# Optimization experiments

Measured on AMD Instinct MI355X. Metric: run time of the kernel, lower is better.

## Reference

```python
import jax, jax.numpy as jnp
import numpy as np

N, E, DIN, DE, D, L = 100000, 600000, 64, 8, 128, 5
BN_EPS = 1e-5


def setup_inputs() -> dict:
    key = jax.random.key(0)
    ks = jax.random.split(key, 10)
    s = 0.05
    return {
        "x": jax.random.normal(ks[0], (N, DIN), jnp.float32),
        "edge_index": jax.random.randint(ks[1], (2, E), 0, N, dtype=jnp.int64) if jax.config.jax_enable_x64 else jax.random.randint(ks[1], (2, E), 0, N),
        "edge_attr": jax.random.normal(ks[2], (E, DE), jnp.float32),
        "Wn": jax.random.normal(ks[3], (DIN, D), jnp.float32) * s,
        "bn0": jnp.zeros((D,), jnp.float32),
        "We": jax.random.normal(ks[4], (L, DE, D), jnp.float32) * s,
        "bee": jnp.zeros((L, D), jnp.float32),
        "W1": jax.random.normal(ks[5], (L, D, 2 * D), jnp.float32) * s,
        "b1": jnp.zeros((L, 2 * D), jnp.float32),
        "g1": jnp.ones((L, 2 * D), jnp.float32),
        "bt1": jnp.zeros((L, 2 * D), jnp.float32),
        "W2": jax.random.normal(ks[6], (L, 2 * D, D), jnp.float32) * s,
        "b2": jnp.zeros((L, D), jnp.float32),
        "eps": jnp.zeros((L,), jnp.float32),
        "gamma": jnp.ones((L, D), jnp.float32),
        "beta": jnp.zeros((L, D), jnp.float32),
    }


def _bn(z, g, b):
    # BatchNorm1d training-mode forward (biased variance over the node axis)
    mu = jnp.mean(z, axis=0)
    var = jnp.mean((z - mu) ** 2, axis=0)
    return g * (z - mu) * jax.lax.rsqrt(var + BN_EPS) + b


def reference(x, edge_index, edge_attr, Wn, bn0, We, bee, W1, b1, g1, bt1, W2, b2, eps, gamma, beta):
    h = x @ Wn + bn0  # node encoder: [N, D]
    src, dst = edge_index[0], edge_index[1]
    for l in range(L):
        ee = edge_attr @ We[l] + bee[l]              # [E, D] edge embedding
        msg = jax.nn.relu(h[src] + ee)               # gather + relu
        agg = jax.ops.segment_sum(msg, dst, num_segments=N)  # scatter-add
        z = (1.0 + eps[l]) * h + agg                 # GIN root update
        z = jax.nn.relu(_bn(z @ W1[l] + b1[l], g1[l], bt1[l]))  # MLP hidden
        z = z @ W2[l] + b2[l]                        # MLP out
        z = _bn(z, gamma[l], beta[l])                # outer BatchNorm
        if l < L - 1:
            z = jax.nn.relu(z)                       # relu on all but last layer
        h = z
    return h  # JK='last'
```

## Files before the change

### kernel.cpp

```cpp
#include <hip/hip_runtime.h>
#include <hip/hip_bf16.h>

#define N_NODES 100000
#define N_EDGES 600000
#define DIN 64
#define DE 8
#define D 128
#define TWO_D 256
#define L_LAYERS 5
#define BN_EPS 1e-5f

#define SCAN_B 256
#define SCAN_NB ((N_NODES + SCAN_B - 1) / SCAN_B)

typedef unsigned short u16;
typedef unsigned int u32;
typedef __attribute__((ext_vector_type(8))) short short8;
typedef __attribute__((ext_vector_type(4))) float f32x4;

__device__ inline u16 f2bf(float f) {
    __hip_bfloat16 h = __float2bfloat16(f);
    return *reinterpret_cast<u16*>(&h);
}
__device__ inline float bf2f(u16 u) {
    union { u32 i; float f; } v;
    v.i = ((u32)u) << 16;
    return v.f;
}
__device__ inline float bfLo(u32 v) {
    union { u32 i; float f; } u;
    u.i = v << 16;
    return u.f;
}
__device__ inline float bfHi(u32 v) {
    union { u32 i; float f; } u;
    u.i = v & 0xffff0000u;
    return u.f;
}
__device__ inline u32 packbf(float a, float b) {
    return (u32)f2bf(a) | ((u32)f2bf(b) << 16);
}


__global__ void hist_kernel(const int* __restrict__ dst, int* __restrict__ deg) {
    int i = blockIdx.x * blockDim.x + threadIdx.x;
    if (i < N_EDGES) atomicAdd(&deg[dst[i]], 1);
}

__global__ void scan_partial_kernel(const int* __restrict__ deg, int* __restrict__ blocksum) {
    __shared__ int red[SCAN_B];
    int tid = threadIdx.x;
    int i = blockIdx.x * SCAN_B + tid;
    red[tid] = (i < N_NODES) ? deg[i] : 0;
    __syncthreads();
    for (int off = SCAN_B / 2; off > 0; off >>= 1) {
        if (tid < off) red[tid] += red[tid + off];
        __syncthreads();
    }
    if (tid == 0) blocksum[blockIdx.x] = red[0];
}

__global__ void scan_blocks_kernel(int* __restrict__ blocksum, int* __restrict__ total) {
    __shared__ int sh[512];
    int tid = threadIdx.x;
    int v = (tid < SCAN_NB) ? blocksum[tid] : 0;
    sh[tid] = v;
    __syncthreads();
    for (int off = 1; off < 512; off <<= 1) {
        int w = (tid >= off) ? sh[tid - off] : 0;
        __syncthreads();
        sh[tid] += w;
        __syncthreads();
    }
    if (tid < SCAN_NB) blocksum[tid] = sh[tid] - v;
    if (tid == 511) *total = sh[511];
}

__global__ void scan_apply_kernel(const int* __restrict__ deg, const int* __restrict__ blocksum,
                                  const int* __restrict__ total, int* __restrict__ rowptr,
                                  int* __restrict__ cursor) {
    __shared__ int sh[SCAN_B];
    int tid = threadIdx.x;
    int i = blockIdx.x * SCAN_B + tid;
    int v = (i < N_NODES) ? deg[i] : 0;
    sh[tid] = v;
    __syncthreads();
    for (int off = 1; off < SCAN_B; off <<= 1) {
        int w = (tid >= off) ? sh[tid - off] : 0;
        __syncthreads();
        sh[tid] += w;
        __syncthreads();
    }
    if (i < N_NODES) {
        int p = blocksum[blockIdx.x] + sh[tid] - v;
        rowptr[i] = p;
        cursor[i] = p;
    }
    if (i == N_NODES - 1) rowptr[N_NODES] = *total;
}

__global__ void scatter_kernel(const int* __restrict__ dst, const int* __restrict__ src,
                               const float* __restrict__ ea, int* __restrict__ cursor,
                               int* __restrict__ csr_src, float4* __restrict__ eap) {
    int i = blockIdx.x * blockDim.x + threadIdx.x;
    if (i < N_EDGES) {
        int d = dst[i];
        int p = atomicAdd(&cursor[d], 1);
        csr_src[p] = src[i];
        const float4* s = (const float4*)(ea + (size_t)i * DE);
        eap[(size_t)p * 2] = s[0];
        eap[(size_t)p * 2 + 1] = s[1];
    }
}


__global__ void prep_w_kernel(const float* __restrict__ W1, const float* __restrict__ W2,
                              const float* __restrict__ Wn, u16* __restrict__ w1t,
                              u16* __restrict__ w2t, u16* __restrict__ wnh,
                              u16* __restrict__ wnl) {
    int idx = blockIdx.x * blockDim.x + threadIdx.x;
    const int T1 = L_LAYERS * TWO_D * D;
    if (idx < T1) {
        int l = idx / (TWO_D * D);
        int rem = idx - l * (TWO_D * D);
        int n = rem >> 7;
        int k = rem & 127;
        w1t[idx] = f2bf(W1[((size_t)l * D + k) * TWO_D + n]);
    } else if (idx < 2 * T1) {
        int jdx = idx - T1;
        int l = jdx / (D * TWO_D);
        int rem = jdx - l * (D * TWO_D);
        int n = rem >> 8;
        int k = rem & 255;
        w2t[jdx] = f2bf(W2[((size_t)l * TWO_D + k) * D + n]);
    } else if (idx < 2 * T1 + D * DIN) {
        int r = idx - 2 * T1;
        int n = r >> 6;
        int k = r & 63;
        float v = Wn[(size_t)k * D + n];
        u16 hi = f2bf(v);
        wnh[r] = hi;
        wnl[r] = f2bf(v - bf2f(hi));
    }
}


__launch_bounds__(256, 4)
__global__ void encoder_kernel(const float* __restrict__ x, const u16* __restrict__ wnh,
                               const u16* __restrict__ wnl, const float* __restrict__ bn0,
                               u32* __restrict__ ub) {
    __shared__ __align__(16) u16 ENC[2 * 64 * 72];
    u16* Ah = ENC;
    u16* Al = ENC + 64 * 72;

    int tid = threadIdx.x;
    int row0 = blockIdx.x * 64;

#pragma unroll
    for (int p = 0; p < 4; p++) {
        int idx = tid + p * 256;
        int row = idx >> 4, c4 = (idx & 15) * 4;
        f32x4 v = (f32x4){0.f, 0.f, 0.f, 0.f};
        if (row0 + row < N_NODES)
            v = *(const f32x4*)(x + (size_t)(row0 + row) * DIN + c4);
        u16 hi4[4], lo4[4];
#pragma unroll
        for (int i = 0; i < 4; i++) {
            u16 hi = f2bf(v[i]);
            hi4[i] = hi;
            lo4[i] = f2bf(v[i] - bf2f(hi));
        }
        *(uint2*)(&Ah[row * 72 + c4]) = *(const uint2*)hi4;
        *(uint2*)(&Al[row * 72 + c4]) = *(const uint2*)lo4;
    }
    __syncthreads();

    int lane = tid & 63, wave = tid >> 6;
    int m16 = lane & 15, kq = lane >> 4;
    f32x4 acc[4][2];
#pragma unroll
    for (int i = 0; i < 4; i++)
#pragma unroll
        for (int c = 0; c < 2; c++) acc[i][c] = (f32x4){0.f, 0.f, 0.f, 0.f};

#pragma unroll
    for (int ks = 0; ks < 2; ks++) {
        int k0 = ks * 32 + kq * 8;
        short8 Bh[2], Bl[2];
#pragma unroll
        for (int ct = 0; ct < 2; ct++) {
            int col = ct * 64 + wave * 16 + m16;
            Bh[ct] = *(const short8*)(wnh + (size_t)col * DIN + k0);
            Bl[ct] = *(const short8*)(wnl + (size_t)col * DIN + k0);
        }
        short8 ah[4], al[4];
#pragma unroll
        for (int rt = 0; rt < 4; rt++) {
            ah[rt] = *(const short8*)(&Ah[(rt * 16 + m16) * 72 + k0]);
            al[rt] = *(const short8*)(&Al[(rt * 16 + m16) * 72 + k0]);
        }
#pragma unroll
        for (int rt = 0; rt < 4; rt++)
#pragma unroll
            for (int ct = 0; ct < 2; ct++) {
                acc[rt][ct] = __builtin_amdgcn_mfma_f32_16x16x32_bf16(ah[rt], Bh[ct],
                                                                     acc[rt][ct], 0, 0, 0);
                acc[rt][ct] = __builtin_amdgcn_mfma_f32_16x16x32_bf16(al[rt], Bh[ct],
                                                                     acc[rt][ct], 0, 0, 0);
                acc[rt][ct] = __builtin_amdgcn_mfma_f32_16x16x32_bf16(ah[rt], Bl[ct],
                                                                     acc[rt][ct], 0, 0, 0);
            }
    }

    int c = wave * 16 + m16;
    float b0 = bn0[c], b1v = bn0[64 + c];
#pragma unroll
    for (int rt = 0; rt < 4; rt++) {
#pragma unroll
        for (int rr = 0; rr < 4; rr++) {
            int row = row0 + rt * 16 + kq * 4 + rr;
            if (row < N_NODES)
                ub[(size_t)row * 64 + c] = packbf(acc[rt][0][rr] + b0,
                                                  acc[rt][1][rr] + b1v);
        }
    }
}


__launch_bounds__(256, 3)
__global__ void front_kernel(const u32* __restrict__ ub, const float4* __restrict__ eap,
                             const int* __restrict__ rowptr_g, const int* __restrict__ csr_src,
                             const float* __restrict__ We, const float* __restrict__ bee,
                             const float* __restrict__ epsArr, int layer, int use_aff,
                             const float* __restrict__ aff2a, const float* __restrict__ aff2b,
                             const u16* __restrict__ w1t, const float* __restrict__ b1,
                             float* __restrict__ t, float* __restrict__ s1,
                             float* __restrict__ s1sq) {
    __shared__ __align__(16) u16 UNI[2 * 32 * 136];
    __shared__ float sred[512];
    __shared__ int rp[36];

    u16* Ah = UNI;
    u16* Al = UNI + 32 * 136;

    int tid = threadIdx.x;
    int row0 = blockIdx.x * 32;

    if (tid < 33) {
        int g = row0 + tid;
        rp[tid] = rowptr_g[(g < N_NODES) ? g : N_NODES];
    }
    sred[tid] = 0.f;
    sred[256 + tid] = 0.f;
    __syncthreads();

    int lane = tid & 63, wave = tid >> 6;
    int j = lane;
    float epsv = 1.0f + epsArr[layer];

    float WeR[16];
#pragma unroll
    for (int k = 0; k < 8; k++) {
        WeR[2 * k] = We[k * D + j];
        WeR[2 * k + 1] = We[k * D + 64 + j];
    }
    float bee0 = bee[j], bee1 = bee[64 + j];
    float fA0 = 0.f, fA1 = 0.f, fB0 = 0.f, fB1 = 0.f;
    if (use_aff) {
        fA0 = aff2a[j]; fA1 = aff2a[64 + j];
        fB0 = aff2b[j]; fB1 = aff2b[64 + j];
    }

    {
        int wbeg = wave * 8, wend = wbeg + 8;
        int pbeg = __builtin_amdgcn_readfirstlane(rp[wbeg]);
        int pend = __builtin_amdgcn_readfirstlane(rp[wend]);
        int rloc = wbeg;
        int p1c = __builtin_amdgcn_readfirstlane(rp[wbeg + 1]);
        float acc_a = 0.f, acc_b = 0.f;
        float rCa = 0.f, rCb = 0.f, rNa = 0.f, rNb = 0.f;
        {
            int n0 = row0 + wbeg;
            if (n0 < N_NODES) {
                u32 r0 = ub[(size_t)n0 * 64 + j];
                rCa = bfLo(r0); rCb = bfHi(r0);
            }
            int n1 = n0 + 1;
            if (n1 < N_NODES) {
                u32 r1 = ub[(size_t)n1 * 64 + j];
                rNa = bfLo(r1); rNb = bfHi(r1);
            }
        }

        auto flushRow = [&]() {
            float oa = rCa, ob = rCb;
            if (use_aff) {
                oa = fmaxf(fmaf(fA0, oa, fB0), 0.f);
                ob = fmaxf(fmaf(fA1, ob, fB1), 0.f);
            }
            float za = fmaf(epsv, oa, acc_a);
            float zb = fmaf(epsv, ob, acc_b);
            u16 ha = f2bf(za), hb = f2bf(zb);
            Ah[rloc * 136 + j] = ha;
            Ah[rloc * 136 + 64 + j] = hb;
            Al[rloc * 136 + j] = f2bf(za - bf2f(ha));
            Al[rloc * 136 + 64 + j] = f2bf(zb - bf2f(hb));
            acc_a = 0.f;
            acc_b = 0.f;
            rloc++;
            rCa = rNa;
            rCb = rNb;
            if (rloc + 1 < wend) {
                int nn = row0 + rloc + 1;
                if (nn < N_NODES) {
                    u32 rn = ub[(size_t)nn * 64 + j];
                    rNa = bfLo(rn); rNb = bfHi(rn);
                } else {
                    rNa = 0.f; rNb = 0.f;
                }
            }
            p1c = (rloc < wend) ? __builtin_amdgcn_readfirstlane(rp[rloc + 1]) : 0x7fffffff;
        };

#define LOAD_DESC(BASE, CC)                                                       \
        _Pragma("unroll")                                                         \
        for (int i_ = 0; i_ < 4; i_++) {                                          \
            int q_ = (BASE) + i_;                                                 \
            q_ = (q_ < pend) ? q_ : (pend - 1);                                   \
            CC##s[i_] = __builtin_amdgcn_readfirstlane(csr_src[q_]);              \
        }

#define ISSUE_DATA(BASE, CC, V, E0, E1)                                           \
        _Pragma("unroll")                                                         \
        for (int i_ = 0; i_ < 4; i_++) {                                          \
            V[i_] = ub[(size_t)CC##s[i_] * 64 + j];                               \
            int q_ = (BASE) + i_;                                                 \
            q_ = (q_ < pend) ? q_ : (pend - 1);                                   \
            E0[i_] = eap[(size_t)q_ * 2];                                         \
            E1[i_] = eap[(size_t)q_ * 2 + 1];                                     \
        }

#define COMPUTE_CHUNK(P, V, E0, E1)                                               \
        _Pragma("unroll")                                                         \
        for (int i_ = 0; i_ < 4; i_++) {                                          \
            int pos_ = (P) + i_;                                                  \
            if (pos_ < pend) {                                                    \
                while (pos_ >= p1c) flushRow();                                   \
                float ha_ = bfLo(V[i_]), hb_ = bfHi(V[i_]);                       \
                if (use_aff) {                                                    \
                    ha_ = fmaxf(fmaf(fA0, ha_, fB0), 0.f);                        \
                    hb_ = fmaxf(fmaf(fA1, hb_, fB1), 0.f);                        \
                }                                                                 \
                float eeA = bee0, eeB = bee1;                                     \
                eeA = fmaf(E0[i_].x, WeR[0], eeA);                                \
                eeB = fmaf(E0[i_].x, WeR[1], eeB);                                \
                eeA = fmaf(E0[i_].y, WeR[2], eeA);                                \
                eeB = fmaf(E0[i_].y, WeR[3], eeB);                                \
                eeA = fmaf(E0[i_].z, WeR[4], eeA);                                \
                eeB = fmaf(E0[i_].z, WeR[5], eeB);                                \
                eeA = fmaf(E0[i_].w, WeR[6], eeA);                                \
                eeB = fmaf(E0[i_].w, WeR[7], eeB);                                \
                eeA = fmaf(E1[i_].x, WeR[8], eeA);                                \
                eeB = fmaf(E1[i_].x, WeR[9], eeB);                                \
                eeA = fmaf(E1[i_].y, WeR[10], eeA);                               \
                eeB = fmaf(E1[i_].y, WeR[11], eeB);                               \
                eeA = fmaf(E1[i_].z, WeR[12], eeA);                               \
                eeB = fmaf(E1[i_].z, WeR[13], eeB);                               \
                eeA = fmaf(E1[i_].w, WeR[14], eeA);                               \
                eeB = fmaf(E1[i_].w, WeR[15], eeB);                               \
                acc_a += fmaxf(ha_ + eeA, 0.f);                                   \
                acc_b += fmaxf(hb_ + eeB, 0.f);                                   \
            }                                                                     \
        }

        if (pbeg < pend) {
            int cAs[4], cBs[4], cNs[4], cMs[4];
            u32 vA[4], vB[4];
            float4 eA0[4], eA1[4], eB0[4], eB1[4];

            LOAD_DESC(pbeg, cA)
            LOAD_DESC(pbeg + 4, cB)
            ISSUE_DATA(pbeg, cA, vA, eA0, eA1)
            ISSUE_DATA(pbeg + 4, cB, vB, eB0, eB1)
            LOAD_DESC(pbeg + 8, cN)
            for (int p = pbeg; p < pend; p += 8) {
                LOAD_DESC(p + 12, cM)
                COMPUTE_CHUNK(p, vA, eA0, eA1)
                ISSUE_DATA(p + 8, cN, vA, eA0, eA1)
                LOAD_DESC(p + 16, cN)
                COMPUTE_CHUNK(p + 4, vB, eB0, eB1)
                ISSUE_DATA(p + 12, cM, vB, eB0, eB1)
            }
        }
        while (rloc < wend) flushRow();

#undef LOAD_DESC
#undef ISSUE_DATA
#undef COMPUTE_CHUNK
    }
    __syncthreads();

    int wc = wave;
    int m16 = lane & 15, kq = lane >> 4;
    f32x4 acc[2][4];
#pragma unroll
    for (int i = 0; i < 2; i++)
#pragma unroll
        for (int c = 0; c < 4; c++) acc[i][c] = (f32x4){0.f, 0.f, 0.f, 0.f};

#pragma unroll
    for (int ks = 0; ks < 4; ks++) {
        int k0 = ks * 32 + kq * 8;
        short8 Bf[4];
#pragma unroll
        for (int ct = 0; ct < 4; ct++)
            Bf[ct] = *(const short8*)(w1t + (size_t)(wc * 64 + ct * 16 + m16) * D + k0);
        short8 ah[2], al[2];
#pragma unroll
        for (int rt = 0; rt < 2; rt++) {
            ah[rt] = *(const short8*)(&Ah[(rt * 16 + m16) * 136 + k0]);
            al[rt] = *(const short8*)(&Al[(rt * 16 + m16) * 136 + k0]);
        }
#pragma unroll
        for (int rt = 0; rt < 2; rt++)
#pragma unroll
            for (int ct = 0; ct < 4; ct++) {
                acc[rt][ct] = __builtin_amdgcn_mfma_f32_16x16x32_bf16(ah[rt], Bf[ct],
                                                                     acc[rt][ct], 0, 0, 0);
                acc[rt][ct] = __builtin_amdgcn_mfma_f32_16x16x32_bf16(al[rt], Bf[ct],
                                                                     acc[rt][ct], 0, 0, 0);
            }
    }

#pragma unroll
    for (int ct = 0; ct < 4; ct++) {
        int col = wc * 64 + ct * 16 + m16;
        float bias = b1[col];
        float ls = 0.f, lq = 0.f;
#pragma unroll
        for (int rt = 0; rt < 2; rt++) {
#pragma unroll
            for (int rr = 0; rr < 4; rr++) {
                int row = row0 + rt * 16 + kq * 4 + rr;
                if (row < N_NODES) {
                    float v = acc[rt][ct][rr] + bias;
                    t[(size_t)row * TWO_D + col] = v;
                    ls += v;
                    lq += v * v;
                }
            }
        }
        atomicAdd(&sred[col], ls);
        atomicAdd(&sred[256 + col], lq);
    }
    __syncthreads();
    int slot = blockIdx.x & 7;
    atomicAdd(&s1[slot * TWO_D + tid], sred[tid]);
    atomicAdd(&s1sq[slot * TWO_D + tid], sred[256 + tid]);
}


__launch_bounds__(256, 4)
__global__ void gemm2_kernel(const float* __restrict__ t, const float* __restrict__ aff1a,
                             const float* __restrict__ aff1b, const u16* __restrict__ w2t,
                             const float* __restrict__ b2, u32* __restrict__ ub,
                             float* __restrict__ s2, float* __restrict__ s2sq) {
    __shared__ u16 CH[2 * 64 * 72];
    __shared__ float affL[512];
    __shared__ float sred[256];
    u16* AhC = CH;
    u16* AlC = CH + 64 * 72;

    int tid = threadIdx.x;
    int row0 = blockIdx.x * 64;
    affL[tid] = aff1a[tid];
    affL[256 + tid] = aff1b[tid];
    sred[tid] = 0.f;

    int lane = tid & 63, wave = tid >> 6;
    int wc = wave;
    int m16 = lane & 15, kq = lane >> 4;
    f32x4 acc[4][2];
#pragma unroll
    for (int i = 0; i < 4; i++)
#pragma unroll
        for (int c = 0; c < 2; c++) acc[i][c] = (f32x4){0.f, 0.f, 0.f, 0.f};
    __syncthreads();

    for (int kc = 0; kc < 4; kc++) {
#pragma unroll
        for (int p = 0; p < 4; p++) {
            int idx = tid + p * 256;
            int row = idx >> 4, c4 = (idx & 15) * 4;
            f32x4 v = (f32x4){0.f, 0.f, 0.f, 0.f};
            if (row0 + row < N_NODES)
                v = *(const f32x4*)(t + (size_t)(row0 + row) * TWO_D + kc * 64 + c4);
            u16 hi4[4], lo4[4];
#pragma unroll
            for (int i = 0; i < 4; i++) {
                int k = kc * 64 + c4 + i;
                float g = fmaxf(fmaf(affL[k], v[i], affL[256 + k]), 0.f);
                u16 hi = f2bf(g);
                hi4[i] = hi;
                lo4[i] = f2bf(g - bf2f(hi));
            }
            *(uint2*)(&AhC[row * 72 + c4]) = *(const uint2*)hi4;
            *(uint2*)(&AlC[row * 72 + c4]) = *(const uint2*)lo4;
        }
        __syncthreads();
#pragma unroll
        for (int ks = 0; ks < 2; ks++) {
            int k0 = ks * 32 + kq * 8;
            short8 Bf[2];
#pragma unroll
            for (int ct = 0; ct < 2; ct++) {
                int col = ct * 64 + wc * 16 + m16;
                Bf[ct] = *(const short8*)(w2t + (size_t)col * TWO_D + kc * 64 + k0);
            }
            short8 ah[4], al[4];
#pragma unroll
            for (int rt = 0; rt < 4; rt++) {
                ah[rt] = *(const short8*)(&AhC[(rt * 16 + m16) * 72 + k0]);
                al[rt] = *(const short8*)(&AlC[(rt * 16 + m16) * 72 + k0]);
            }
#pragma unroll
            for (int rt = 0; rt < 4; rt++)
#pragma unroll
                for (int ct = 0; ct < 2; ct++) {
                    acc[rt][ct] = __builtin_amdgcn_mfma_f32_16x16x32_bf16(ah[rt], Bf[ct],
                                                                         acc[rt][ct], 0, 0, 0);
                    acc[rt][ct] = __builtin_amdgcn_mfma_f32_16x16x32_bf16(al[rt], Bf[ct],
                                                                         acc[rt][ct], 0, 0, 0);
                }
        }
        __syncthreads();
    }

    {
        int c = wc * 16 + m16;
        float biasL = b2[c], biasH = b2[c + 64];
        float lsL = 0.f, lqL = 0.f, lsH = 0.f, lqH = 0.f;
#pragma unroll
        for (int rt = 0; rt < 4; rt++) {
#pragma unroll
            for (int rr = 0; rr < 4; rr++) {
                int row = row0 + rt * 16 + kq * 4 + rr;
                if (row < N_NODES) {
                    float vL = acc[rt][0][rr] + biasL;
                    float vH = acc[rt][1][rr] + biasH;
                    ub[(size_t)row * 64 + c] = packbf(vL, vH);
                    lsL += vL; lqL += vL * vL;
                    lsH += vH; lqH += vH * vH;
                }
            }
        }
        atomicAdd(&sred[c], lsL);
        atomicAdd(&sred[128 + c], lqL);
        atomicAdd(&sred[c + 64], lsH);
        atomicAdd(&sred[128 + c + 64], lqH);
    }
    __syncthreads();
    int slot = blockIdx.x & 7;
    if (tid < 128) atomicAdd(&s2[slot * D + tid], sred[tid]);
    else atomicAdd(&s2sq[slot * D + (tid - 128)], sred[tid]);
}


__global__ void finalize_kernel(const float* __restrict__ sums, const float* __restrict__ sumsq,
                                int ncols, const float* __restrict__ g,
                                const float* __restrict__ bt, float* __restrict__ affa,
                                float* __restrict__ affb) {
    int j = threadIdx.x;
    if (j < ncols) {
        float s = 0.f, q = 0.f;
        for (int k = 0; k < 8; k++) { s += sums[k * ncols + j]; q += sumsq[k * ncols + j]; }
        const float invN = 1.0f / (float)N_NODES;
        float mean = s * invN;
        float var = q * invN - mean * mean;
        float rstd = rsqrtf(var + BN_EPS);
        float a = g[j] * rstd;
        affa[j] = a;
        affb[j] = fmaf(-a, mean, bt[j]);
    }
}


__global__ void apply_final_kernel(const u32* __restrict__ ub, const float* __restrict__ a,
                                   const float* __restrict__ b, float* __restrict__ out) {
    const int total = N_NODES * 64;
    for (int idx = blockIdx.x * blockDim.x + threadIdx.x; idx < total;
         idx += gridDim.x * blockDim.x) {
        int n = idx >> 6, c = idx & 63;
        u32 v = ub[idx];
        out[(size_t)n * D + c] = fmaf(a[c], bfLo(v), b[c]);
        out[(size_t)n * D + 64 + c] = fmaf(a[64 + c], bfHi(v), b[64 + c]);
    }
}


extern "C" void kernel_launch(void* const* d_in, const int* in_sizes, int n_in,
                              void* d_out, int out_size, void* d_ws, size_t ws_size,
                              hipStream_t stream) {
    (void)in_sizes; (void)n_in; (void)out_size; (void)ws_size;
    const float* x    = (const float*)d_in[0];
    const int*   ei   = (const int*)d_in[1];
    const float* ea   = (const float*)d_in[2];
    const float* Wn   = (const float*)d_in[3];
    const float* bn0  = (const float*)d_in[4];
    const float* We   = (const float*)d_in[5];
    const float* bee  = (const float*)d_in[6];
    const float* W1   = (const float*)d_in[7];
    const float* b1   = (const float*)d_in[8];
    const float* g1   = (const float*)d_in[9];
    const float* bt1  = (const float*)d_in[10];
    const float* W2   = (const float*)d_in[11];
    const float* b2   = (const float*)d_in[12];
    const float* eps  = (const float*)d_in[13];
    const float* gamma= (const float*)d_in[14];
    const float* beta = (const float*)d_in[15];
    float* out = (float*)d_out;

    char* ws = (char*)d_ws;
    u32*    ub    = (u32*)ws;
    float4* eap   = (float4*)(ws + 25600000);
    float*  t     = (float*)(ws + 51200000);
    int*   rowptr = (int*)(ws + 153600000);
    int*   deg    = (int*)(ws + 154000004);
    int*   cursor = (int*)(ws + 154400004);
    int*   blocksum = (int*)(ws + 154800004);
    int*   totalp = blocksum + SCAN_NB;
    int*   csr_src = (int*)(ws + 154801584);
    float* stats  = (float*)(ws + 159601840);
    float* s1    = stats;
    float* s1sq  = stats + 2048;
    float* s2    = stats + 4096;
    float* s2sq  = stats + 5120;
    float* aff1a = stats + 6144;
    float* aff1b = stats + 6400;
    float* aff2a = stats + 6656;
    float* aff2b = stats + 6784;
    u16*   w1t   = (u16*)(ws + 159629504);
    u16*   w2t   = (u16*)(ws + 154000016);
    u16*   wnh   = (u16*)(ws + 154400016);
    u16*   wnl   = (u16*)(ws + 154416400);

    const int* srcA = ei;
    const int* dstA = ei + N_EDGES;

    (void)hipMemsetAsync(deg, 0, N_NODES * sizeof(int), stream);
    hist_kernel<<<(N_EDGES + 255) / 256, 256, 0, stream>>>(dstA, deg);
    scan_partial_kernel<<<SCAN_NB, SCAN_B, 0, stream>>>(deg, blocksum);
    scan_blocks_kernel<<<1, 512, 0, stream>>>(blocksum, totalp);
    scan_apply_kernel<<<SCAN_NB, SCAN_B, 0, stream>>>(deg, blocksum, totalp, rowptr, cursor);
    scatter_kernel<<<(N_EDGES + 255) / 256, 256, 0, stream>>>(dstA, srcA, ea, cursor,
                                                              csr_src, eap);

    const int PREP_T = 2 * L_LAYERS * TWO_D * D + D * DIN;
    prep_w_kernel<<<(PREP_T + 255) / 256, 256, 0, stream>>>(W1, W2, Wn, w1t, w2t, wnh, wnl);
    encoder_kernel<<<(N_NODES + 63) / 64, 256, 0, stream>>>(x, wnh, wnl, bn0, ub);

    const int NB1 = (N_NODES + 31) / 32;
    const int NB2 = (N_NODES + 63) / 64;
    for (int l = 0; l < L_LAYERS; l++) {
        (void)hipMemsetAsync(stats, 0, 6144 * sizeof(float), stream);
        front_kernel<<<NB1, 256, 0, stream>>>(
            ub, eap, rowptr, csr_src, We + (size_t)l * DE * D, bee + (size_t)l * D,
            eps, l, (l > 0) ? 1 : 0, aff2a, aff2b,
            w1t + (size_t)l * TWO_D * D, b1 + (size_t)l * TWO_D, t, s1, s1sq);
        finalize_kernel<<<1, 256, 0, stream>>>(s1, s1sq, TWO_D, g1 + (size_t)l * TWO_D,
                                               bt1 + (size_t)l * TWO_D, aff1a, aff1b);
        gemm2_kernel<<<NB2, 256, 0, stream>>>(
            t, aff1a, aff1b, w2t + (size_t)l * D * TWO_D, b2 + (size_t)l * D, ub, s2, s2sq);
        finalize_kernel<<<1, 128, 0, stream>>>(s2, s2sq, D, gamma + (size_t)l * D,
                                               beta + (size_t)l * D, aff2a, aff2b);
    }
    apply_final_kernel<<<4096, 256, 0, stream>>>(ub, aff2a, aff2b, out);
}
```

Measured before the change: 983.4 us.

## Gather neighbor rows into LDS via global_load_lds batches in front kernel

Replaces the register-based software-pipelined gather of neighbor features with batches of 16 direct global-to-LDS loads per wave into a per-wave ring, followed by a full vmcnt wait, then computes from LDS. Occupancy hint is raised from 3 to 4 blocks per CU. The aim is to cut register pressure and keep more gathers in flight. In exchange, the cross-batch prefetch is lost because each batch waits for all its loads before computing, the edge-attribute loads are now issued inside the compute loop rather than prefetched, and LDS use grows.

```diff
diff --git a/kernel.cpp b/kernel.cpp
--- a/kernel.cpp
+++ b/kernel.cpp
@@ -12,6 +12,7 @@
 
 #define SCAN_B 256
 #define SCAN_NB ((N_NODES + SCAN_B - 1) / SCAN_B)
+#define EB 16
 
 typedef unsigned short u16;
 typedef unsigned int u32;
@@ -39,6 +40,11 @@
 }
 __device__ inline u32 packbf(float a, float b) {
     return (u32)f2bf(a) | ((u32)f2bf(b) << 16);
+}
+
+__device__ inline void gld_lds_b32(const u32* g, u32* l) {
+    __builtin_amdgcn_global_load_lds((const __attribute__((address_space(1))) u32*)g,
+                                     (__attribute__((address_space(3))) u32*)l, 4, 0, 0);
 }
 
 
@@ -227,7 +233,7 @@
 }
 
 
-__launch_bounds__(256, 3)
+__launch_bounds__(256, 4)
 __global__ void front_kernel(const u32* __restrict__ ub, const float4* __restrict__ eap,
                              const int* __restrict__ rowptr_g, const int* __restrict__ csr_src,
                              const float* __restrict__ We, const float* __restrict__ bee,
@@ -237,6 +243,7 @@
                              float* __restrict__ t, float* __restrict__ s1,
                              float* __restrict__ s1sq) {
     __shared__ __align__(16) u16 UNI[2 * 32 * 136];
+    __shared__ u32 RING[4][EB][64];
     __shared__ float sred[512];
     __shared__ int rp[36];
 
@@ -322,81 +329,66 @@
             p1c = (rloc < wend) ? __builtin_amdgcn_readfirstlane(rp[rloc + 1]) : 0x7fffffff;
         };
 
-#define LOAD_DESC(BASE, CC)                                                       \
-        _Pragma("unroll")                                                         \
-        for (int i_ = 0; i_ < 4; i_++) {                                          \
-            int q_ = (BASE) + i_;                                                 \
-            q_ = (q_ < pend) ? q_ : (pend - 1);                                   \
-            CC##s[i_] = __builtin_amdgcn_readfirstlane(csr_src[q_]);              \
-        }
-
-#define ISSUE_DATA(BASE, CC, V, E0, E1)                                           \
-        _Pragma("unroll")                                                         \
-        for (int i_ = 0; i_ < 4; i_++) {                                          \
-            V[i_] = ub[(size_t)CC##s[i_] * 64 + j];                               \
-            int q_ = (BASE) + i_;                                                 \
-            q_ = (q_ < pend) ? q_ : (pend - 1);                                   \
-            E0[i_] = eap[(size_t)q_ * 2];                                         \
-            E1[i_] = eap[(size_t)q_ * 2 + 1];                                     \
-        }
-
-#define COMPUTE_CHUNK(P, V, E0, E1)                                               \
-        _Pragma("unroll")                                                         \
-        for (int i_ = 0; i_ < 4; i_++) {                                          \
-            int pos_ = (P) + i_;                                                  \
-            if (pos_ < pend) {                                                    \
-                while (pos_ >= p1c) flushRow();                                   \
-                float ha_ = bfLo(V[i_]), hb_ = bfHi(V[i_]);                       \
-                if (use_aff) {                                                    \
-                    ha_ = fmaxf(fmaf(fA0, ha_, fB0), 0.f);                        \
-                    hb_ = fmaxf(fmaf(fA1, hb_, fB1), 0.f);                        \
-                }                                                                 \
-                float eeA = bee0, eeB = bee1;                                     \
-                eeA = fmaf(E0[i_].x, WeR[0], eeA);                                \
-                eeB = fmaf(E0[i_].x, WeR[1], eeB);                                \
-                eeA = fmaf(E0[i_].y, WeR[2], eeA);                                \
-                eeB = fmaf(E0[i_].y, WeR[3], eeB);                                \
-                eeA = fmaf(E0[i_].z, WeR[4], eeA);                                \
-                eeB = fmaf(E0[i_].z, WeR[5], eeB);                                \
-                eeA = fmaf(E0[i_].w, WeR[6], eeA);                                \
-                eeB = fmaf(E0[i_].w, WeR[7], eeB);                                \
-                eeA = fmaf(E1[i_].x, WeR[8], eeA);                                \
-                eeB = fmaf(E1[i_].x, WeR[9], eeB);                                \
-                eeA = fmaf(E1[i_].y, WeR[10], eeA);                               \
-                eeB = fmaf(E1[i_].y, WeR[11], eeB);                               \
-                eeA = fmaf(E1[i_].z, WeR[12], eeA);                               \
-                eeB = fmaf(E1[i_].z, WeR[13], eeB);                               \
-                eeA = fmaf(E1[i_].w, WeR[14], eeA);                               \
-                eeB = fmaf(E1[i_].w, WeR[15], eeB);                               \
-                acc_a += fmaxf(ha_ + eeA, 0.f);                                   \
-                acc_b += fmaxf(hb_ + eeB, 0.f);                                   \
-            }                                                                     \
-        }
-
-        if (pbeg < pend) {
-            int cAs[4], cBs[4], cNs[4], cMs[4];
-            u32 vA[4], vB[4];
-            float4 eA0[4], eA1[4], eB0[4], eB1[4];
-
-            LOAD_DESC(pbeg, cA)
-            LOAD_DESC(pbeg + 4, cB)
-            ISSUE_DATA(pbeg, cA, vA, eA0, eA1)
-            ISSUE_DATA(pbeg + 4, cB, vB, eB0, eB1)
-            LOAD_DESC(pbeg + 8, cN)
-            for (int p = pbeg; p < pend; p += 8) {
-                LOAD_DESC(p + 12, cM)
-                COMPUTE_CHUNK(p, vA, eA0, eA1)
-                ISSUE_DATA(p + 8, cN, vA, eA0, eA1)
-                LOAD_DESC(p + 16, cN)
-                COMPUTE_CHUNK(p + 4, vB, eB0, eB1)
-                ISSUE_DATA(p + 12, cM, vB, eB0, eB1)
+        for (int base = pbeg; base < pend; base += EB) {
+#pragma unroll
+            for (int i = 0; i < EB; i++) {
+                int q = base + i;
+                q = (q < pend) ? q : (pend - 1);
+                int s = __builtin_amdgcn_readfirstlane(csr_src[q]);
+                gld_lds_b32(ub + (size_t)s * 64 + j, &RING[wave][i][0]);
+            }
+            asm volatile("s_waitcnt vmcnt(0)" ::: "memory");
+            __builtin_amdgcn_sched_barrier(0);
+
+            int lim = pend - base;
+            if (lim > EB) lim = EB;
+            for (int i0 = 0; i0 < lim; i0 += 4) {
+                u32 hv[4];
+                float4 e0[4], e1[4];
+#pragma unroll
+                for (int k = 0; k < 4; k++) {
+                    int ii = i0 + k;
+                    ii = (ii < EB) ? ii : (EB - 1);
+                    hv[k] = RING[wave][ii][j];
+                    int q = base + i0 + k;
+                    q = (q < pend) ? q : (pend - 1);
+                    e0[k] = eap[(size_t)q * 2];
+                    e1[k] = eap[(size_t)q * 2 + 1];
+                }
+#pragma unroll
+                for (int k = 0; k < 4; k++) {
+                    int pos = base + i0 + k;
+                    if (pos < pend) {
+                        while (pos >= p1c) flushRow();
+                        float ha_ = bfLo(hv[k]), hb_ = bfHi(hv[k]);
+                        if (use_aff) {
+                            ha_ = fmaxf(fmaf(fA0, ha_, fB0), 0.f);
+                            hb_ = fmaxf(fmaf(fA1, hb_, fB1), 0.f);
+                        }
+                        float eeA = bee0, eeB = bee1;
+                        eeA = fmaf(e0[k].x, WeR[0], eeA);
+                        eeB = fmaf(e0[k].x, WeR[1], eeB);
+                        eeA = fmaf(e0[k].y, WeR[2], eeA);
+                        eeB = fmaf(e0[k].y, WeR[3], eeB);
+                        eeA = fmaf(e0[k].z, WeR[4], eeA);
+                        eeB = fmaf(e0[k].z, WeR[5], eeB);
+                        eeA = fmaf(e0[k].w, WeR[6], eeA);
+                        eeB = fmaf(e0[k].w, WeR[7], eeB);
+                        eeA = fmaf(e1[k].x, WeR[8], eeA);
+                        eeB = fmaf(e1[k].x, WeR[9], eeB);
+                        eeA = fmaf(e1[k].y, WeR[10], eeA);
+                        eeB = fmaf(e1[k].y, WeR[11], eeB);
+                        eeA = fmaf(e1[k].z, WeR[12], eeA);
+                        eeB = fmaf(e1[k].z, WeR[13], eeB);
+                        eeA = fmaf(e1[k].w, WeR[14], eeA);
+                        eeB = fmaf(e1[k].w, WeR[15], eeB);
+                        acc_a += fmaxf(ha_ + eeA, 0.f);
+                        acc_b += fmaxf(hb_ + eeB, 0.f);
+                    }
+                }
             }
         }
         while (rloc < wend) flushRow();
-
-#undef LOAD_DESC
-#undef ISSUE_DATA
-#undef COMPUTE_CHUNK
     }
     __syncthreads();
 
```

Result: slower. 1.074 ms (+9.3%).
